# Kernel tuning notes

Measured on AMD Instinct MI355X. Metric: run time of the kernel, lower is better.

The kernel has to match this reference:

```python
import jax, jax.numpy as jnp
import numpy as np

D, H, DFF, K, S = 512, 8, 2048, 4, 4
DH = D // H
SHAPES = [(56, 56), (28, 28), (14, 14), (7, 7)]
B = 4


def setup_inputs() -> dict:
    key = jax.random.key(0)
    ks = jax.random.split(key, 32)
    inp = {}
    for i, (hl, wl) in enumerate(SHAPES):
        inp[f'src{i}'] = jax.random.normal(ks[i], (B, hl, wl, D), jnp.float32)
        inp[f'ref{i}'] = jax.random.uniform(ks[4 + i], (B, hl, wl, 2), jnp.float32)
    def lin(k, fan_in, fan_out):
        return jax.random.normal(k, (fan_in, fan_out), jnp.float32) * (1.0 / np.sqrt(fan_in))
    inp['Wv'] = lin(ks[8], D, D)
    inp['bv'] = jnp.zeros((D,), jnp.float32)
    inp['Woff'] = jax.random.normal(ks[9], (D, H * S * K * 2), jnp.float32) * 0.01
    inp['boff'] = jax.random.normal(ks[10], (H * S * K * 2,), jnp.float32) * 0.1
    inp['Wattn'] = jax.random.normal(ks[11], (D, H * S * K), jnp.float32) * 0.01
    inp['battn'] = jnp.zeros((H * S * K,), jnp.float32)
    inp['Wo'] = lin(ks[12], D, D)
    inp['bo'] = jnp.zeros((D,), jnp.float32)
    inp['W1'] = lin(ks[13], D, DFF)
    inp['b1'] = jnp.zeros((DFF,), jnp.float32)
    inp['W2'] = lin(ks[14], DFF, D)
    inp['b2'] = jnp.zeros((D,), jnp.float32)
    inp['g1'] = jnp.ones((D,), jnp.float32)
    inp['be1'] = jnp.zeros((D,), jnp.float32)
    inp['g2'] = jnp.ones((D,), jnp.float32)
    inp['be2'] = jnp.zeros((D,), jnp.float32)
    return inp


def layernorm(x, g, b, eps=1e-5):
    mu = jnp.mean(x, axis=-1, keepdims=True)
    var = jnp.mean(jnp.square(x - mu), axis=-1, keepdims=True)
    return (x - mu) * jax.lax.rsqrt(var + eps) * g + b


def bilinear_sample(value, loc):
    # value: [B, Hl, Wl, H, DH] per-scale projected values; loc: [B, Lq, H, K, 2] in [0,1]
    b, hl, wl, h, dh = value.shape
    x = loc[..., 0] * wl - 0.5
    y = loc[..., 1] * hl - 0.5
    x0f = jnp.floor(x); y0f = jnp.floor(y)
    wx1 = x - x0f; wx0 = 1.0 - wx1
    wy1 = y - y0f; wy0 = 1.0 - wy1
    x0 = x0f.astype(jnp.int32); y0 = y0f.astype(jnp.int32)
    vflat = value.transpose(0, 3, 1, 2, 4).reshape(b, h, hl * wl, dh)  # [B,H,HW,DH]

    def corner(xi, yi, w):
        valid = ((xi >= 0) & (xi < wl) & (yi >= 0) & (yi < hl)).astype(value.dtype)
        idx = jnp.clip(yi, 0, hl - 1) * wl + jnp.clip(xi, 0, wl - 1)  # [B,Lq,H,K]
        idx = idx.transpose(0, 2, 1, 3)  # [B,H,Lq,K]
        lq, kk = idx.shape[2], idx.shape[3]
        g = jnp.take_along_axis(vflat, idx.reshape(b, h, lq * kk)[..., None], axis=2)
        g = g.reshape(b, h, lq, kk, dh)
        wv = (w * valid).transpose(0, 2, 1, 3)[..., None]  # [B,H,Lq,K,1]
        return g * wv

    out = (corner(x0, y0, wx0 * wy0) + corner(x0 + 1, y0, wx1 * wy0)
           + corner(x0, y0 + 1, wx0 * wy1) + corner(x0 + 1, y0 + 1, wx1 * wy1))
    return out.transpose(0, 2, 1, 3, 4)  # [B,Lq,H,K,DH]


def _forward(src0, src1, src2, src3, ref0, ref1, ref2, ref3,
             Wv, bv, Woff, boff, Wattn, battn, Wo, bo, W1, b1, W2, b2, g1, be1, g2, be2):
    srcs = [src0, src1, src2, src3]
    refs = [ref0, ref1, ref2, ref3]
    # shared value projection per scale, split into heads
    values = [(s @ Wv + bv).reshape(s.shape[0], s.shape[1], s.shape[2], H, DH) for s in srcs]
    outs = []
    for src_l, ref_l in zip(srcs, refs):
        b = src_l.shape[0]
        q = src_l.reshape(b, -1, D)          # [B,Lq,D]
        ref = ref_l.reshape(b, -1, 2)        # [B,Lq,2]
        lq = q.shape[1]
        off = (q @ Woff + boff).reshape(b, lq, H, S, K, 2)
        attn = jax.nn.softmax((q @ Wattn + battn).reshape(b, lq, H, S * K), axis=-1)
        attn = attn.reshape(b, lq, H, S, K)
        acc = jnp.zeros((b, lq, H, DH), q.dtype)
        for li, (v, (hl, wl)) in enumerate(zip(values, SHAPES)):
            scale = jnp.array([wl, hl], q.dtype)
            loc = ref[:, :, None, None, :] + off[:, :, :, li] / scale  # [B,Lq,H,K,2]
            samp = bilinear_sample(v, loc)                              # [B,Lq,H,K,DH]
            acc = acc + jnp.einsum('blhk,blhkd->blhd', attn[:, :, :, li], samp)
        a = acc.reshape(b, lq, D) @ Wo + bo
        x = layernorm(q + a, g1, be1)
        f = jax.nn.relu(x @ W1 + b1) @ W2 + b2
        x = layernorm(x + f, g2, be2)
        outs.append(x)
    return jnp.concatenate(outs, axis=1)  # [B, sum(Hl*Wl), D]


def reference(src0, src1, src2, src3, ref0, ref1, ref2, ref3,
              Wv, bv, Woff, boff, Wattn, battn, Wo, bo, W1, b1, W2, b2, g1, be1, g2, be2):
    return _forward(src0, src1, src2, src3, ref0, ref1, ref2, ref3,
                    Wv, bv, Woff, boff, Wattn, battn, Wo, bo, W1, b1, W2, b2, g1, be1, g2, be2)
```

## Files before the change

### kernel.cpp

```cpp
#include <hip/hip_runtime.h>
#include <math.h>


#define TTOT 16660
#define TPAD 16768
#define LQTOT 4165

typedef __attribute__((ext_vector_type(8))) short bf16x8;
typedef __attribute__((ext_vector_type(4))) float f32x4;

typedef __attribute__((address_space(1))) const unsigned int g_u32;
typedef __attribute__((address_space(3))) unsigned int l_u32;

__device__ __forceinline__ unsigned short f2bf(float f) {
    unsigned u = __builtin_bit_cast(unsigned, f);
    u += 0x7fffu + ((u >> 16) & 1u);
    return (unsigned short)(u >> 16);
}
__device__ __forceinline__ float bf2f(unsigned short s) {
    unsigned u = ((unsigned)s) << 16;
    return __builtin_bit_cast(float, u);
}
__device__ __forceinline__ float bflo(unsigned u) {
    return __builtin_bit_cast(float, u << 16);
}
__device__ __forceinline__ float bfhi(unsigned u) {
    return __builtin_bit_cast(float, u & 0xffff0000u);
}

__device__ __forceinline__ int permute_row(int t) {
    int off, area, qoff;
    if (t < 12544)      { off = 0;     area = 3136; qoff = 0;    }
    else if (t < 15680) { off = 12544; area = 784;  qoff = 3136; }
    else if (t < 16464) { off = 15680; area = 196;  qoff = 3920; }
    else                { off = 16464; area = 49;   qoff = 4116; }
    int rel = t - off;
    int b = rel / area;
    int pos = rel - b * area;
    return b * LQTOT + qoff + pos;
}

__device__ __forceinline__ const float* src_row(int row, const float* s0, const float* s1,
                                                const float* s2, const float* s3) {
    if (row < 12544) return s0 + (size_t)row * 512;
    if (row < 15680) return s1 + (size_t)(row - 12544) * 512;
    if (row < 16464) return s2 + (size_t)(row - 15680) * 512;
    return s3 + (size_t)(row - 16464) * 512;
}

__device__ __forceinline__ void async_copy16(const unsigned short* g, unsigned short* lds_wave_uniform) {
    __builtin_amdgcn_global_load_lds((g_u32*)g, (l_u32*)lds_wave_uniform, 16, 0, 0);
}

enum { EPI_SPLIT = 0, EPI_RESID_SRC = 1, EPI_RELU = 2, EPI_RESID_SCATTER = 3 };

struct GemmArgs {
    const unsigned short* A;
    const unsigned short* Bt;
    const float* bias0; const float* bias1; const float* bias2;
    const unsigned short* residb;
    const float* s0; const float* s1; const float* s2; const float* s3;
    void* out0; unsigned short* out1; unsigned short* out2;
    int M, N, Kd;
};

template <int EPI>
__global__ __launch_bounds__(256) void gemm_mfma(GemmArgs a)
{
    __shared__ unsigned short As[128 * 64];
    __shared__ unsigned short Bs[128 * 64];
    const int tid  = threadIdx.x;
    const int wave = tid >> 6;
    const int lane = tid & 63;
    const int m0 = blockIdx.y * 128;
    const int n0 = blockIdx.x * 128;

    const int srow = tid >> 3;
    const int kg   = (tid & 7) ^ (srow & 7);
    const unsigned short* Ag = a.A  + (size_t)(m0 + srow) * a.Kd + kg * 8;
    const unsigned short* Bg = a.Bt + (size_t)(n0 + srow) * a.Kd + kg * 8;
    const size_t rstep32 = (size_t)32 * a.Kd;
    unsigned short* ldsA = As + wave * 512;
    unsigned short* ldsB = Bs + wave * 512;

    const int wm = (wave >> 1) << 6;
    const int wn = (wave & 1) << 6;
    const int fm = lane & 15;
    const int fq = lane >> 4;
    const int fx7 = fm & 7;

    const f32x4 fzero = {0.f, 0.f, 0.f, 0.f};
    f32x4 acc[4][4];
#pragma unroll
    for (int i = 0; i < 4; ++i)
#pragma unroll
        for (int j = 0; j < 4; ++j) acc[i][j] = fzero;

    for (int k0 = 0; k0 < a.Kd; k0 += 64) {
        __syncthreads();
#pragma unroll
        for (int p = 0; p < 4; ++p) {
            async_copy16(Ag + p * rstep32 + k0, ldsA + p * 2048);
            async_copy16(Bg + p * rstep32 + k0, ldsB + p * 2048);
        }
        __syncthreads();
#pragma unroll
        for (int sub = 0; sub < 2; ++sub) {
            const int slot = ((sub * 4 + fq) ^ fx7) << 3;
            bf16x8 af[4], bfr[4];
#pragma unroll
            for (int mt = 0; mt < 4; ++mt)
                af[mt] = *(const bf16x8*)&As[(wm + mt * 16 + fm) * 64 + slot];
#pragma unroll
            for (int nt = 0; nt < 4; ++nt)
                bfr[nt] = *(const bf16x8*)&Bs[(wn + nt * 16 + fm) * 64 + slot];
#pragma unroll
            for (int mt = 0; mt < 4; ++mt)
#pragma unroll
                for (int nt = 0; nt < 4; ++nt)
                    acc[mt][nt] = __builtin_amdgcn_mfma_f32_16x16x32_bf16(
                        af[mt], bfr[nt], acc[mt][nt], 0, 0, 0);
        }
    }

    const int cn0 = n0 + wn + fm;
    int cols[4]; float bi[4];
#pragma unroll
    for (int nt = 0; nt < 4; ++nt) {
        const int c = cn0 + nt * 16;
        cols[nt] = c;
        if (EPI == EPI_SPLIT)
            bi[nt] = (c < 512) ? a.bias0[c] : (c < 768) ? a.bias1[c - 512] : a.bias2[c - 768];
        else
            bi[nt] = a.bias0[c];
    }
#pragma unroll
    for (int mt = 0; mt < 4; ++mt) {
#pragma unroll
        for (int r = 0; r < 4; ++r) {
            const int row = m0 + wm + mt * 16 + fq * 4 + r;
            if (row >= a.M) continue;
            const size_t ro = (size_t)row;
            const float* srcres = (EPI == EPI_RESID_SRC)
                                  ? src_row(row, a.s0, a.s1, a.s2, a.s3) : nullptr;
#pragma unroll
            for (int nt = 0; nt < 4; ++nt) {
                float v = acc[mt][nt][r] + bi[nt];
                const int c = cols[nt];
                if (EPI == EPI_SPLIT) {
                    if (c < 512)      ((unsigned short*)a.out0)[ro * 512 + c]        = f2bf(v);
                    else if (c < 768) a.out1[ro * 256 + (c - 512)]                   = f2bf(v);
                    else              a.out2[ro * 128 + (c - 768)]                   = f2bf(v);
                } else if (EPI == EPI_RESID_SRC) {
                    v += srcres[c];
                    ((unsigned short*)a.out0)[ro * 512 + c] = f2bf(v);
                } else if (EPI == EPI_RELU) {
                    v = fmaxf(v, 0.f);
                    ((unsigned short*)a.out0)[ro * 2048 + c] = f2bf(v);
                } else {
                    v += bf2f(a.residb[ro * 512 + c]);
                    ((float*)a.out0)[(size_t)permute_row(row) * 512 + c] = v;
                }
            }
        }
    }
}

struct PrepArgs {
    const float *Wv, *Woff, *Wattn, *Wo, *W1, *W2;
    unsigned short *Wcat, *Wot, *W1t, *W2t;
    const float *s0, *s1, *s2, *s3;
    unsigned short* Qb;
};

__global__ __launch_bounds__(256) void prep(PrepArgs p)
{
    __shared__ unsigned short t[32][33];
    const int bid = blockIdx.x;
    if (bid < 2752) {
        const float* W; unsigned short* Wt; int K, N, lbx, rel;
        if (bid < 256)       { W = p.Wv;    Wt = p.Wcat;                   K = 512;  N = 512;  lbx = 4; rel = bid; }
        else if (bid < 384)  { W = p.Woff;  Wt = p.Wcat + (size_t)512*512; K = 512;  N = 256;  lbx = 3; rel = bid - 256; }
        else if (bid < 448)  { W = p.Wattn; Wt = p.Wcat + (size_t)768*512; K = 512;  N = 128;  lbx = 2; rel = bid - 384; }
        else if (bid < 704)  { W = p.Wo;    Wt = p.Wot;                    K = 512;  N = 512;  lbx = 4; rel = bid - 448; }
        else if (bid < 1728) { W = p.W1;    Wt = p.W1t;                    K = 512;  N = 2048; lbx = 6; rel = bid - 704; }
        else                 { W = p.W2;    Wt = p.W2t;                    K = 2048; N = 512;  lbx = 4; rel = bid - 1728; }
        const int bx = rel & ((1 << lbx) - 1);
        const int by = rel >> lbx;
        const int tx = threadIdx.x & 31, ty = threadIdx.x >> 5;
        const int nb = bx * 32, kb = by * 32;
#pragma unroll
        for (int j = 0; j < 32; j += 8)
            t[ty + j][tx] = f2bf(W[(size_t)(kb + ty + j) * N + nb + tx]);
        __syncthreads();
#pragma unroll
        for (int j = 0; j < 32; j += 8)
            Wt[(size_t)(nb + ty + j) * K + kb + tx] = t[tx][ty + j];
    } else {
        const int gid = (bid - 2752) * 256 + threadIdx.x;
        const int e = gid * 4;
        const int row = e >> 9, col = e & 511;
        const float* sr = src_row(row, p.s0, p.s1, p.s2, p.s3);
        const float4 v = *(const float4*)(sr + col);
        ushort4 o;
        o.x = f2bf(v.x); o.y = f2bf(v.y); o.z = f2bf(v.z); o.w = f2bf(v.w);
        *(ushort4*)(p.Qb + (size_t)row * 512 + col) = o;
    }
}

__global__ __launch_bounds__(256) void sample_attn(
    const unsigned short* __restrict__ Vp, const unsigned short* __restrict__ OFFB,
    const unsigned short* __restrict__ ATT,
    const float* __restrict__ rf0, const float* __restrict__ rf1,
    const float* __restrict__ rf2, const float* __restrict__ rf3,
    unsigned short* __restrict__ ACCb)
{
    __shared__ int   midx[4][8][17][4];
    __shared__ float mw[4][8][17][4];
    const int tid = threadIdx.x;

#pragma unroll
    for (int i = 0; i < 2; ++i) {
        const int slot = i * 256 + tid;
        const int tl = slot >> 7;
        const int h  = (slot >> 4) & 7;
        const int s  = slot & 15;
        const int t  = blockIdx.x * 4 + tl;
        const int li = s >> 2;

        int soff, area;
        const float* rp;
        if (t < 12544)      { soff = 0;     area = 3136; rp = rf0 + (size_t)t * 2; }
        else if (t < 15680) { soff = 12544; area = 784;  rp = rf1 + (size_t)(t - 12544) * 2; }
        else if (t < 16464) { soff = 15680; area = 196;  rp = rf2 + (size_t)(t - 15680) * 2; }
        else                { soff = 16464; area = 49;   rp = rf3 + (size_t)(t - 16464) * 2; }
        const int b = (t - soff) / area;

        float logit = bf2f(ATT[(size_t)t * 128 + h * 16 + s]);
        float mx = logit;
#pragma unroll
        for (int o = 8; o > 0; o >>= 1) mx = fmaxf(mx, __shfl_xor(mx, o, 16));
        float e = __expf(logit - mx);
        float sumv = e;
#pragma unroll
        for (int o = 8; o > 0; o >>= 1) sumv += __shfl_xor(sumv, o, 16);
        const float ew = e / sumv;

        const int wl = 56 >> li;
        const int lvlbase = (li == 0) ? 0 : (li == 1) ? 12544 : (li == 2) ? 15680 : 16464;
        const int base = lvlbase + b * wl * wl;
        const float rx = rp[0], ry = rp[1];
        const unsigned off2 = *(const unsigned*)(OFFB + (size_t)t * 256 + h * 32 + s * 2);
        const float ox = bflo(off2);
        const float oy = bfhi(off2);
        const float x = rx * (float)wl + ox - 0.5f;
        const float y = ry * (float)wl + oy - 0.5f;
        const float x0f = floorf(x), y0f = floorf(y);
        const float wx1 = x - x0f, wx0 = 1.f - wx1;
        const float wy1 = y - y0f, wy0 = 1.f - wy1;
        const int x0 = (int)x0f, y0 = (int)y0f;
        const int x1 = x0 + 1, y1 = y0 + 1;
        const int xc0 = min(max(x0, 0), wl - 1), xc1 = min(max(x1, 0), wl - 1);
        const int yc0 = min(max(y0, 0), wl - 1), yc1 = min(max(y1, 0), wl - 1);
        const float fx0 = (x0 >= 0 && x0 < wl) ? 1.f : 0.f;
        const float fx1 = (x1 >= 0 && x1 < wl) ? 1.f : 0.f;
        const float fy0 = (y0 >= 0 && y0 < wl) ? 1.f : 0.f;
        const float fy1 = (y1 >= 0 && y1 < wl) ? 1.f : 0.f;
        const int hb2 = h * 128;
        int4 I;
        I.x = (base + yc0 * wl + xc0) * 1024 + hb2;
        I.y = (base + yc0 * wl + xc1) * 1024 + hb2;
        I.z = (base + yc1 * wl + xc0) * 1024 + hb2;
        I.w = (base + yc1 * wl + xc1) * 1024 + hb2;
        float4 Wt;
        Wt.x = wx0 * wy0 * fx0 * fy0 * ew;
        Wt.y = wx1 * wy0 * fx1 * fy0 * ew;
        Wt.z = wx0 * wy1 * fx0 * fy1 * ew;
        Wt.w = wx1 * wy1 * fx1 * fy1 * ew;
        *(int4*)&midx[tl][h][s][0] = I;
        *(float4*)&mw[tl][h][s][0] = Wt;
    }
    __syncthreads();

    const int wave = tid >> 6;
    const int lane = tid & 63;
    const int tl = wave;
    const int h  = lane >> 3;
    const int t  = blockIdx.x * 4 + tl;
    const int off16 = (lane & 7) * 16;
    const char* vb = (const char*)Vp;
    float a0 = 0.f, a1 = 0.f, a2 = 0.f, a3 = 0.f;
    float a4 = 0.f, a5 = 0.f, a6 = 0.f, a7 = 0.f;
#pragma unroll
    for (int s = 0; s < 16; ++s) {
        const int4   I = *(const int4*)&midx[tl][h][s][0];
        const float4 W = *(const float4*)&mw[tl][h][s][0];
        const uint4 u0 = *(const uint4*)(vb + (I.x + off16));
        const uint4 u1 = *(const uint4*)(vb + (I.y + off16));
        const uint4 u2 = *(const uint4*)(vb + (I.z + off16));
        const uint4 u3 = *(const uint4*)(vb + (I.w + off16));
        a0 += W.x * bflo(u0.x); a1 += W.x * bfhi(u0.x); a2 += W.x * bflo(u0.y); a3 += W.x * bfhi(u0.y);
        a4 += W.x * bflo(u0.z); a5 += W.x * bfhi(u0.z); a6 += W.x * bflo(u0.w); a7 += W.x * bfhi(u0.w);
        a0 += W.y * bflo(u1.x); a1 += W.y * bfhi(u1.x); a2 += W.y * bflo(u1.y); a3 += W.y * bfhi(u1.y);
        a4 += W.y * bflo(u1.z); a5 += W.y * bfhi(u1.z); a6 += W.y * bflo(u1.w); a7 += W.y * bfhi(u1.w);
        a0 += W.z * bflo(u2.x); a1 += W.z * bfhi(u2.x); a2 += W.z * bflo(u2.y); a3 += W.z * bfhi(u2.y);
        a4 += W.z * bflo(u2.z); a5 += W.z * bfhi(u2.z); a6 += W.z * bflo(u2.w); a7 += W.z * bfhi(u2.w);
        a0 += W.w * bflo(u3.x); a1 += W.w * bfhi(u3.x); a2 += W.w * bflo(u3.y); a3 += W.w * bfhi(u3.y);
        a4 += W.w * bflo(u3.z); a5 += W.w * bfhi(u3.z); a6 += W.w * bflo(u3.w); a7 += W.w * bfhi(u3.w);
    }
    uint4 o;
    o.x = ((unsigned)f2bf(a1) << 16) | f2bf(a0);
    o.y = ((unsigned)f2bf(a3) << 16) | f2bf(a2);
    o.z = ((unsigned)f2bf(a5) << 16) | f2bf(a4);
    o.w = ((unsigned)f2bf(a7) << 16) | f2bf(a6);
    *(uint4*)((char*)ACCb + (size_t)t * 1024 + h * 128 + off16) = o;
}

__global__ __launch_bounds__(256) void ln_bf16(
    unsigned short* __restrict__ X, const float* __restrict__ g, const float* __restrict__ be)
{
    const int row = blockIdx.x;
    unsigned short* xr = X + (size_t)row * 512;
    const int tid = threadIdx.x;
    float v0 = bf2f(xr[tid]);
    float v1 = bf2f(xr[tid + 256]);
    float s = v0 + v1;
    float ss = v0 * v0 + v1 * v1;
#pragma unroll
    for (int o = 32; o > 0; o >>= 1) {
        s += __shfl_down(s, o, 64);
        ss += __shfl_down(ss, o, 64);
    }
    __shared__ float sm[4], sm2[4];
    const int w = tid >> 6;
    if ((tid & 63) == 0) { sm[w] = s; sm2[w] = ss; }
    __syncthreads();
    if (tid == 0) {
        sm[0] = sm[0] + sm[1] + sm[2] + sm[3];
        sm2[0] = sm2[0] + sm2[1] + sm2[2] + sm2[3];
    }
    __syncthreads();
    const float mu = sm[0] * (1.f / 512.f);
    const float var = sm2[0] * (1.f / 512.f) - mu * mu;
    const float rs = rsqrtf(var + 1e-5f);
    xr[tid]       = f2bf((v0 - mu) * rs * g[tid]       + be[tid]);
    xr[tid + 256] = f2bf((v1 - mu) * rs * g[tid + 256] + be[tid + 256]);
}

__global__ __launch_bounds__(256) void ln_f32(
    float* __restrict__ X, const float* __restrict__ g, const float* __restrict__ be)
{
    const int row = blockIdx.x;
    float* xr = X + (size_t)row * 512;
    const int tid = threadIdx.x;
    float v0 = xr[tid];
    float v1 = xr[tid + 256];
    float s = v0 + v1;
    float ss = v0 * v0 + v1 * v1;
#pragma unroll
    for (int o = 32; o > 0; o >>= 1) {
        s += __shfl_down(s, o, 64);
        ss += __shfl_down(ss, o, 64);
    }
    __shared__ float sm[4], sm2[4];
    const int w = tid >> 6;
    if ((tid & 63) == 0) { sm[w] = s; sm2[w] = ss; }
    __syncthreads();
    if (tid == 0) {
        sm[0] = sm[0] + sm[1] + sm[2] + sm[3];
        sm2[0] = sm2[0] + sm2[1] + sm2[2] + sm2[3];
    }
    __syncthreads();
    const float mu = sm[0] * (1.f / 512.f);
    const float var = sm2[0] * (1.f / 512.f) - mu * mu;
    const float rs = rsqrtf(var + 1e-5f);
    xr[tid]       = (v0 - mu) * rs * g[tid]       + be[tid];
    xr[tid + 256] = (v1 - mu) * rs * g[tid + 256] + be[tid + 256];
}

extern "C" void kernel_launch(void* const* d_in, const int* in_sizes, int n_in,
                              void* d_out, int out_size, void* d_ws, size_t ws_size,
                              hipStream_t stream)
{
    const float* src[4] = { (const float*)d_in[0], (const float*)d_in[2],
                            (const float*)d_in[4], (const float*)d_in[6] };
    const float* ref[4] = { (const float*)d_in[1], (const float*)d_in[3],
                            (const float*)d_in[5], (const float*)d_in[7] };
    const float* Wv    = (const float*)d_in[8];
    const float* bv    = (const float*)d_in[9];
    const float* Woff  = (const float*)d_in[10];
    const float* boff  = (const float*)d_in[11];
    const float* Wattn = (const float*)d_in[12];
    const float* battn = (const float*)d_in[13];
    const float* Wo    = (const float*)d_in[14];
    const float* bo    = (const float*)d_in[15];
    const float* W1    = (const float*)d_in[16];
    const float* b1    = (const float*)d_in[17];
    const float* W2    = (const float*)d_in[18];
    const float* b2    = (const float*)d_in[19];
    const float* g1    = (const float*)d_in[20];
    const float* be1   = (const float*)d_in[21];
    const float* g2    = (const float*)d_in[22];
    const float* be2   = (const float*)d_in[23];

    unsigned short* w    = (unsigned short*)d_ws;
    unsigned short* Qb   = w;
    unsigned short* Vp   = Qb   + (size_t)TPAD * 512;
    unsigned short* OFFB = Vp   + (size_t)TPAD * 512;
    unsigned short* ATT  = OFFB + (size_t)TPAD * 256;
    unsigned short* ACCb = ATT  + (size_t)TPAD * 128;
    unsigned short* X1b  = ACCb + (size_t)TPAD * 512;
    unsigned short* Fb   = X1b  + (size_t)TPAD * 512;
    unsigned short* Wcat = Fb   + (size_t)TPAD * 2048;
    unsigned short* Wot  = Wcat + (size_t)896 * 512;
    unsigned short* W1t  = Wot  + (size_t)512 * 512;
    unsigned short* W2t  = W1t  + (size_t)2048 * 512;

    const dim3 blk(256);

    PrepArgs pp = {};
    pp.Wv = Wv; pp.Woff = Woff; pp.Wattn = Wattn; pp.Wo = Wo; pp.W1 = W1; pp.W2 = W2;
    pp.Wcat = Wcat; pp.Wot = Wot; pp.W1t = W1t; pp.W2t = W2t;
    pp.s0 = src[0]; pp.s1 = src[1]; pp.s2 = src[2]; pp.s3 = src[3];
    pp.Qb = Qb;
    prep<<<dim3(11082), blk, 0, stream>>>(pp);

    GemmArgs a1 = {};
    a1.A = Qb; a1.Bt = Wcat; a1.bias0 = bv; a1.bias1 = boff; a1.bias2 = battn;
    a1.out0 = Vp; a1.out1 = OFFB; a1.out2 = ATT; a1.M = TTOT; a1.N = 896; a1.Kd = 512;
    gemm_mfma<EPI_SPLIT><<<dim3(7, 131), blk, 0, stream>>>(a1);

    sample_attn<<<dim3(TTOT / 4), blk, 0, stream>>>(Vp, OFFB, ATT,
                                                    ref[0], ref[1], ref[2], ref[3], ACCb);

    GemmArgs a2 = {};
    a2.A = ACCb; a2.Bt = Wot; a2.bias0 = bo;
    a2.s0 = src[0]; a2.s1 = src[1]; a2.s2 = src[2]; a2.s3 = src[3];
    a2.out0 = X1b; a2.M = TTOT; a2.N = 512; a2.Kd = 512;
    gemm_mfma<EPI_RESID_SRC><<<dim3(4, 131), blk, 0, stream>>>(a2);

    ln_bf16<<<dim3(TTOT), blk, 0, stream>>>(X1b, g1, be1);

    GemmArgs a3 = {};
    a3.A = X1b; a3.Bt = W1t; a3.bias0 = b1;
    a3.out0 = Fb; a3.M = TTOT; a3.N = 2048; a3.Kd = 512;
    gemm_mfma<EPI_RELU><<<dim3(16, 131), blk, 0, stream>>>(a3);

    GemmArgs a4 = {};
    a4.A = Fb; a4.Bt = W2t; a4.bias0 = b2; a4.residb = X1b;
    a4.out0 = d_out; a4.M = TTOT; a4.N = 512; a4.Kd = 2048;
    gemm_mfma<EPI_RESID_SCATTER><<<dim3(4, 131), blk, 0, stream>>>(a4);

    ln_f32<<<dim3(TTOT), blk, 0, stream>>>((float*)d_out, g2, be2);
}
```

Measured before the change: 390.6 us.

## Split-K the FFN down-projection GEMM and fuse partial sum into final layernorm

The 2048-deep W2 GEMM is split into two K halves along a third grid dimension. Each half writes fp32 partials: one into a reused workspace region, the other into the output buffer. The final layernorm now adds both partials and the bf16 residual, using an inverse row permutation to find it. The goal is more blocks for the long-K GEMM and less tail underutilisation, at the cost of extra fp32 partial traffic through memory.

```diff
diff --git a/kernel.cpp b/kernel.cpp
--- a/kernel.cpp
+++ b/kernel.cpp
@@ -40,6 +40,17 @@
     return b * LQTOT + qoff + pos;
 }
 
+__device__ __forceinline__ int inv_permute_row(int r) {
+    int b = r / LQTOT;
+    int pos = r - b * LQTOT;
+    int off, area, qoff;
+    if (pos < 3136)      { off = 0;     area = 3136; qoff = 0;    }
+    else if (pos < 3920) { off = 12544; area = 784;  qoff = 3136; }
+    else if (pos < 4116) { off = 15680; area = 196;  qoff = 3920; }
+    else                 { off = 16464; area = 49;   qoff = 4116; }
+    return off + b * area + (pos - qoff);
+}
+
 __device__ __forceinline__ const float* src_row(int row, const float* s0, const float* s1,
                                                 const float* s2, const float* s3) {
     if (row < 12544) return s0 + (size_t)row * 512;
@@ -52,16 +63,17 @@
     __builtin_amdgcn_global_load_lds((g_u32*)g, (l_u32*)lds_wave_uniform, 16, 0, 0);
 }
 
-enum { EPI_SPLIT = 0, EPI_RESID_SRC = 1, EPI_RELU = 2, EPI_RESID_SCATTER = 3 };
+enum { EPI_SPLIT = 0, EPI_RESID_SRC = 1, EPI_RELU = 2, EPI_PART = 3 };
 
 struct GemmArgs {
     const unsigned short* A;
     const unsigned short* Bt;
     const float* bias0; const float* bias1; const float* bias2;
-    const unsigned short* residb;
     const float* s0; const float* s1; const float* s2; const float* s3;
     void* out0; unsigned short* out1; unsigned short* out2;
+    void* out0b;
     int M, N, Kd;
+    int lda, ldb;
 };
 
 template <int EPI>
@@ -74,12 +86,16 @@
     const int lane = tid & 63;
     const int m0 = blockIdx.y * 128;
     const int n0 = blockIdx.x * 128;
+    const int kc = blockIdx.z;
 
     const int srow = tid >> 3;
     const int kg   = (tid & 7) ^ (srow & 7);
-    const unsigned short* Ag = a.A  + (size_t)(m0 + srow) * a.Kd + kg * 8;
-    const unsigned short* Bg = a.Bt + (size_t)(n0 + srow) * a.Kd + kg * 8;
-    const size_t rstep32 = (size_t)32 * a.Kd;
+    const unsigned short* Ag = a.A  + (size_t)kc * a.Kd
+                             + (size_t)(m0 + srow) * a.lda + kg * 8;
+    const unsigned short* Bg = a.Bt + (size_t)kc * a.Kd
+                             + (size_t)(n0 + srow) * a.ldb + kg * 8;
+    const size_t rstepA = (size_t)32 * a.lda;
+    const size_t rstepB = (size_t)32 * a.ldb;
     unsigned short* ldsA = As + wave * 512;
     unsigned short* ldsB = Bs + wave * 512;
 
@@ -100,8 +116,8 @@
         __syncthreads();
 #pragma unroll
         for (int p = 0; p < 4; ++p) {
-            async_copy16(Ag + p * rstep32 + k0, ldsA + p * 2048);
-            async_copy16(Bg + p * rstep32 + k0, ldsB + p * 2048);
+            async_copy16(Ag + p * rstepA + k0, ldsA + p * 2048);
+            async_copy16(Bg + p * rstepB + k0, ldsB + p * 2048);
         }
         __syncthreads();
 #pragma unroll
@@ -134,6 +150,12 @@
         else
             bi[nt] = a.bias0[c];
     }
+    if (EPI == EPI_PART && kc != 0) {
+#pragma unroll
+        for (int nt = 0; nt < 4; ++nt) bi[nt] = 0.f;
+    }
+    float* pout = (EPI == EPI_PART)
+                ? (float*)(kc ? a.out0b : a.out0) : nullptr;
 #pragma unroll
     for (int mt = 0; mt < 4; ++mt) {
 #pragma unroll
@@ -143,6 +165,7 @@
             const size_t ro = (size_t)row;
             const float* srcres = (EPI == EPI_RESID_SRC)
                                   ? src_row(row, a.s0, a.s1, a.s2, a.s3) : nullptr;
+            const size_t po = (EPI == EPI_PART) ? (size_t)permute_row(row) : 0;
 #pragma unroll
             for (int nt = 0; nt < 4; ++nt) {
                 float v = acc[mt][nt][r] + bi[nt];
@@ -158,8 +181,7 @@
                     v = fmaxf(v, 0.f);
                     ((unsigned short*)a.out0)[ro * 2048 + c] = f2bf(v);
                 } else {
-                    v += bf2f(a.residb[ro * 512 + c]);
-                    ((float*)a.out0)[(size_t)permute_row(row) * 512 + c] = v;
+                    pout[po * 512 + c] = v;
                 }
             }
         }
@@ -347,14 +369,19 @@
     xr[tid + 256] = f2bf((v1 - mu) * rs * g[tid + 256] + be[tid + 256]);
 }
 
-__global__ __launch_bounds__(256) void ln_f32(
-    float* __restrict__ X, const float* __restrict__ g, const float* __restrict__ be)
-{
-    const int row = blockIdx.x;
-    float* xr = X + (size_t)row * 512;
+__global__ __launch_bounds__(256) void ln_final(
+    float* __restrict__ OutD, const float* __restrict__ P0,
+    const unsigned short* __restrict__ X1b,
+    const float* __restrict__ g, const float* __restrict__ be)
+{
+    const int r = blockIdx.x;
+    const int t = inv_permute_row(r);
+    float* xr = OutD + (size_t)r * 512;
+    const float* p0 = P0 + (size_t)r * 512;
+    const unsigned short* res = X1b + (size_t)t * 512;
     const int tid = threadIdx.x;
-    float v0 = xr[tid];
-    float v1 = xr[tid + 256];
+    float v0 = p0[tid]       + xr[tid]       + bf2f(res[tid]);
+    float v1 = p0[tid + 256] + xr[tid + 256] + bf2f(res[tid + 256]);
     float s = v0 + v1;
     float ss = v0 * v0 + v1 * v1;
 #pragma unroll
@@ -415,6 +442,7 @@
     unsigned short* Wot  = Wcat + (size_t)896 * 512;
     unsigned short* W1t  = Wot  + (size_t)512 * 512;
     unsigned short* W2t  = W1t  + (size_t)2048 * 512;
+    float* P0 = (float*)d_ws;
 
     const dim3 blk(256);
 
@@ -427,7 +455,8 @@
 
     GemmArgs a1 = {};
     a1.A = Qb; a1.Bt = Wcat; a1.bias0 = bv; a1.bias1 = boff; a1.bias2 = battn;
-    a1.out0 = Vp; a1.out1 = OFFB; a1.out2 = ATT; a1.M = TTOT; a1.N = 896; a1.Kd = 512;
+    a1.out0 = Vp; a1.out1 = OFFB; a1.out2 = ATT;
+    a1.M = TTOT; a1.N = 896; a1.Kd = 512; a1.lda = 512; a1.ldb = 512;
     gemm_mfma<EPI_SPLIT><<<dim3(7, 131), blk, 0, stream>>>(a1);
 
     sample_attn<<<dim3(TTOT / 4), blk, 0, stream>>>(Vp, OFFB, ATT,
@@ -436,20 +465,21 @@
     GemmArgs a2 = {};
     a2.A = ACCb; a2.Bt = Wot; a2.bias0 = bo;
     a2.s0 = src[0]; a2.s1 = src[1]; a2.s2 = src[2]; a2.s3 = src[3];
-    a2.out0 = X1b; a2.M = TTOT; a2.N = 512; a2.Kd = 512;
+    a2.out0 = X1b; a2.M = TTOT; a2.N = 512; a2.Kd = 512; a2.lda = 512; a2.ldb = 512;
     gemm_mfma<EPI_RESID_SRC><<<dim3(4, 131), blk, 0, stream>>>(a2);
 
     ln_bf16<<<dim3(TTOT), blk, 0, stream>>>(X1b, g1, be1);
 
     GemmArgs a3 = {};
     a3.A = X1b; a3.Bt = W1t; a3.bias0 = b1;
-    a3.out0 = Fb; a3.M = TTOT; a3.N = 2048; a3.Kd = 512;
+    a3.out0 = Fb; a3.M = TTOT; a3.N = 2048; a3.Kd = 512; a3.lda = 512; a3.ldb = 512;
     gemm_mfma<EPI_RELU><<<dim3(16, 131), blk, 0, stream>>>(a3);
 
     GemmArgs a4 = {};
-    a4.A = Fb; a4.Bt = W2t; a4.bias0 = b2; a4.residb = X1b;
-    a4.out0 = d_out; a4.M = TTOT; a4.N = 512; a4.Kd = 2048;
-    gemm_mfma<EPI_RESID_SCATTER><<<dim3(4, 131), blk, 0, stream>>>(a4);
-
-    ln_f32<<<dim3(TTOT), blk, 0, stream>>>((float*)d_out, g2, be2);
-}
+    a4.A = Fb; a4.Bt = W2t; a4.bias0 = b2;
+    a4.out0 = P0; a4.out0b = d_out;
+    a4.M = TTOT; a4.N = 512; a4.Kd = 1024; a4.lda = 2048; a4.ldb = 2048;
+    gemm_mfma<EPI_PART><<<dim3(4, 131, 2), blk, 0, stream>>>(a4);
+
+    ln_final<<<dim3(TTOT), blk, 0, stream>>>((float*)d_out, P0, X1b, g2, be2);
+}
```

Result: no change. 389.4 us (-0.3%).
